# Performance work log

Hardware: AMD Instinct MI355X
Metric: run time of the kernel (lower is better)

The kernel has to match this reference:

```python
import math
import jax, jax.numpy as jnp
import numpy as np

N_HEAD = 16
N_CLUSTER = 64
GROUP_SIZE = 256


def _sinusoidal(n, d):
    # emb[p, 2j] = sin(p*div_j), emb[p, 2j+1] = cos(p*div_j)  (interleaved, as in torch source)
    pos = jnp.arange(n, dtype=jnp.float32)[:, None]
    div = jnp.exp(jnp.arange(0, d, 2, dtype=jnp.float32) * (-math.log(10000.0) / d))
    ang = pos * div  # [n, d//2]
    return jnp.stack([jnp.sin(ang), jnp.cos(ang)], axis=-1).reshape(n, d)


def _rotary(pe, x):
    # Faithful to source: sin = first half of interleaved table, cos = second half,
    # and the function RETURNS ONLY the rotated term (not x*cos + rot*sin).
    d = x.shape[-1]
    sin, cos = pe[..., : d // 2], pe[..., d // 2 :]
    x_even, x_odd = x[..., ::2], x[..., 1::2]
    out = jnp.stack([-x_odd * cos, x_even * sin], axis=-1)
    return out.reshape(jnp.broadcast_shapes(x.shape[:-1] + (d // 2,), out.shape[:-1]) + (2,)).reshape(x.shape) if False else jnp.broadcast_to(out, x.shape[:-1] + (d // 2, 2)).reshape(x.shape)


def _forward(x, w_attn, b_attn, w_proj, b_proj, w_assign):
    B, T, C = x.shape
    H, nc, gs = N_HEAD, N_CLUSTER, GROUP_SIZE
    hd = C // H
    ntpc = T // nc                 # tokens per cluster
    G = T // gs                    # number of groups
    ncpg = gs // ntpc              # clusters summarized per group
    c_max = (G - 1) * ncpg         # max cluster-KV length (padded)

    qkv = x @ w_attn.T + b_attn    # [B, T, 3C]
    q, k, v = jnp.split(qkv, 3, axis=-1)

    # ---- soft cluster summarization (block-diagonal softmax over each cluster's tokens) ----
    x_r = x.reshape(B, nc, ntpc, C)
    logits = jnp.einsum('bctd,cd->bct', x_r, w_assign)        # only diagonal cluster survives the mask
    w = jax.nn.softmax(logits, axis=-1)                        # [B, nc, ntpc]
    ck = jnp.einsum('bct,bctd->bcd', w, k.reshape(B, nc, ntpc, C))  # [B, nc, C]
    cv = jnp.einsum('bct,bctd->bcd', w, v.reshape(B, nc, ntpc, C))

    # ---- split into groups & heads ----
    qg = q.reshape(B, G, gs, H, hd).transpose(0, 1, 3, 2, 4)   # [B,G,H,gs,hd]
    kl = k.reshape(B, G, gs, H, hd).transpose(0, 1, 3, 2, 4)
    vl = v.reshape(B, G, gs, H, hd).transpose(0, 1, 3, 2, 4)
    kc = ck[:, :c_max].reshape(B, c_max, H, hd)                # [B,c_max,H,hd]
    vc = cv[:, :c_max].reshape(B, c_max, H, hd)

    # ---- rotary (positions restart per group; cluster tokens occupy positions 0..c-1) ----
    S = _sinusoidal(c_max + gs, hd)
    qr = _rotary(S[:gs], qg)                                   # q positions 0..gs-1 in every group
    kcr = _rotary(S[:c_max, None, :], kc)                      # cluster slot j -> position j
    pos_local = jnp.arange(G)[:, None] * ncpg + jnp.arange(gs)[None, :]  # [G,gs]
    klr = _rotary(S[pos_local][None, :, None], kl)             # local key p in group g -> pos g*ncpg+p

    # ---- attention: cluster KV (fully visible, masked to first g*ncpg) + local causal ----
    scale = 1.0 / math.sqrt(hd)
    sc = jnp.einsum('bghqd,bchd->bghqc', qr, kcr) * scale      # [B,G,H,gs,c_max]
    sl = jnp.einsum('bghqd,bghkd->bghqk', qr, klr) * scale     # [B,G,H,gs,gs]
    cmask = jnp.arange(c_max)[None, :] < (jnp.arange(G) * ncpg)[:, None]  # [G,c_max]
    sc = jnp.where(cmask[None, :, None, None, :], sc, -jnp.inf)
    lmask = jnp.tril(jnp.ones((gs, gs), dtype=bool))
    sl = jnp.where(lmask, sl, -jnp.inf)
    p = jax.nn.softmax(jnp.concatenate([sc, sl], axis=-1), axis=-1)
    pc, pl = p[..., :c_max], p[..., c_max:]
    y = jnp.einsum('bghqc,bchd->bghqd', pc, vc) + jnp.einsum('bghqk,bghkd->bghqd', pl, vl)
    y = y.transpose(0, 1, 3, 2, 4).reshape(B, T, C)
    return y @ w_proj.T + b_proj


def setup_inputs() -> dict:
    key = jax.random.key(0)
    ks = jax.random.split(key, 4)
    B, T, C, NC = 4, 4096, 1024, N_CLUSTER
    x = jax.random.normal(ks[0], (B, T, C), jnp.float32)
    w_attn = jax.random.normal(ks[1], (3 * C, C), jnp.float32) * 0.02
    b_attn = jnp.zeros((3 * C,), jnp.float32)
    w_proj = jax.random.normal(ks[2], (C, C), jnp.float32) * 0.02
    b_proj = jnp.zeros((C,), jnp.float32)
    w_assign = jax.random.normal(ks[3], (NC, C), jnp.float32) * 0.02
    return {"x": x, "w_attn": w_attn, "b_attn": b_attn, "w_proj": w_proj, "b_proj": b_proj, "w_assign": w_assign}


def reference(x, w_attn, b_attn, w_proj, b_proj, w_assign):
    return _forward(x, w_attn, b_attn, w_proj, b_proj, w_assign)
```

## Files before the change

### kernel.cpp

```cpp
#include <hip/hip_runtime.h>
#include <stdint.h>

typedef unsigned short u16;
typedef unsigned int   u32;
typedef __attribute__((ext_vector_type(8))) short short8;
typedef __attribute__((ext_vector_type(4))) short short4v;
typedef __attribute__((ext_vector_type(4))) float float4v;
typedef __attribute__((ext_vector_type(4))) u32   uint4v;

#define B_  4
#define T_  4096
#define C_  1024
#define H_  16
#define G_  16
#define GS_ 256
#define NC_ 64

static __device__ __forceinline__ u16 f2bf(float f){
  union{float f; u32 u;} c; c.f = f;
  return (u16)((c.u + 0x7fffu + ((c.u >> 16) & 1u)) >> 16);
}
static __device__ __forceinline__ float bf2f(u16 u){
  union{u32 u; float f;} c; c.u = ((u32)u) << 16; return c.f;
}
static __device__ __forceinline__ void gload16(const void* g, void* l){
  __builtin_amdgcn_global_load_lds((__attribute__((address_space(1))) void*)g,
                                   (__attribute__((address_space(3))) void*)l, 16, 0, 0);
}
static __device__ __forceinline__ short8 rot8(short8 v, const float* Sp, int i0){
  union{ short8 s; u32 u[4]; } a, o; a.s = v;
  #pragma unroll
  for(int p = 0; p < 4; p++){
    float e0 = bf2f((u16)(a.u[p] & 0xffffu));
    float e1 = bf2f((u16)(a.u[p] >> 16));
    float sn = Sp[i0 + p], cs = Sp[32 + i0 + p];
    o.u[p] = (u32)f2bf(-e1 * cs) | ((u32)f2bf(e0 * sn) << 16);
  }
  return o.s;
}

__global__ __launch_bounds__(256) void f2b_kernel(const float* __restrict__ s,
                                                  u16* __restrict__ d, int n4){
  int i = blockIdx.x * 256 + threadIdx.x;
  if(i >= n4) return;
  float4v v = *(const float4v*)(s + (size_t)i * 4);
  short4v o;
  o.x = (short)f2bf(v.x); o.y = (short)f2bf(v.y);
  o.z = (short)f2bf(v.z); o.w = (short)f2bf(v.w);
  *(short4v*)(d + (size_t)i * 4) = o;
}

__global__ void stab_kernel(float* __restrict__ S){
  int pos = blockIdx.x, d = threadIdx.x;
  int j = d >> 1;
  float div = expf((float)(2 * j) * (-0.14391156831212787f));
  float ang = (float)pos * div;
  S[pos * 64 + d] = (d & 1) ? cosf(ang) : sinf(ang);
}

template<int MODE>
__global__ __launch_bounds__(512, 1) void gemm8p(const u16* __restrict__ A,
    const u16* __restrict__ Bm, const float* __restrict__ bias,
    void* __restrict__ Cv, u16* __restrict__ vtout, int M, int N, int K, int nbn)
{
  __shared__ u16 sA[2][2][256][32];
  __shared__ u16 sB[2][2][256][32];
  const int tid = threadIdx.x;
  const int lane = tid & 63, w = tid >> 6;
  const int l15 = lane & 15, l4 = lane >> 4;
  const int wr = w >> 2, wc = w & 3;

  const int cpx = gridDim.x >> 3;
  const int bid = blockIdx.x;
  const int swz = (bid & 7) * cpx + (bid >> 3);
  const int bm = swz / nbn, bn = swz - bm * nbn;
  const int row0 = bm * 256, col0 = bn * 256;

  float4v acc[8][4];
  #pragma unroll
  for(int m = 0; m < 8; m++)
    #pragma unroll
    for(int n = 0; n < 4; n++) acc[m][n] = (float4v){0.f, 0.f, 0.f, 0.f};

  const int srow = lane >> 2;
  const int sslot = lane & 3;

  auto stageHalfA = [&](u16* dstPlane, int ktOff){
    #pragma unroll
    for(int l = 0; l < 2; l++){
      int r = w * 32 + l * 16 + srow;
      int ss = sslot ^ ((r >> 1) & 3);
      const u16* src;
      if(MODE == 2){
        int bg = (row0 + r) >> 8;
        int hh = ktOff >> 6;
        int coff = (ktOff & 63) + ss * 8;
        src = A + ((size_t)(bg * 16 + hh)) * 16384 + (size_t)(r & 255) * 64 + coff;
      } else {
        src = A + (size_t)(row0 + r) * K + ktOff + ss * 8;
      }
      gload16(src, dstPlane + (w * 32 + l * 16) * 32);
    }
  };
  auto stageHalfB = [&](u16* dstPlane, int ktOff){
    #pragma unroll
    for(int l = 0; l < 2; l++){
      int r = w * 32 + l * 16 + srow;
      int ss = sslot ^ ((r >> 1) & 3);
      gload16(Bm + (size_t)(col0 + r) * K + ktOff + ss * 8,
              dstPlane + (w * 32 + l * 16) * 32);
    }
  };
  auto ldsReadA = [&](int d, int kk, int mh, short8* af){
    #pragma unroll
    for(int i = 0; i < 4; i++){
      int r = wr * 128 + (mh * 4 + i) * 16 + l15;
      int slot = l4 ^ ((r >> 1) & 3);
      af[i] = *(const short8*)&sA[d][kk][r][slot * 8];
    }
  };
  auto ldsReadB = [&](int d, int kk, short8* bf){
    #pragma unroll
    for(int i = 0; i < 4; i++){
      int r = wc * 64 + i * 16 + l15;
      int slot = l4 ^ ((r >> 1) & 3);
      bf[i] = *(const short8*)&sB[d][kk][r][slot * 8];
    }
  };
  auto mfma16 = [&](int mh, short8* af, short8* bf){
    __builtin_amdgcn_s_setprio(1);
    #pragma unroll
    for(int i = 0; i < 4; i++)
      #pragma unroll
      for(int n = 0; n < 4; n++)
        acc[mh * 4 + i][n] = __builtin_amdgcn_mfma_f32_16x16x32_bf16(af[i], bf[n], acc[mh * 4 + i][n], 0, 0, 0);
    __builtin_amdgcn_s_setprio(0);
  };

  stageHalfA(&sA[0][0][0][0], 0);
  stageHalfB(&sB[0][0][0][0], 0);
  stageHalfA(&sA[0][1][0][0], 32);
  stageHalfB(&sB[0][1][0][0], 32);
  asm volatile("s_waitcnt vmcnt(4)" ::: "memory");
  __builtin_amdgcn_s_barrier();

  const int nT = K >> 6;
  for(int t = 0; t < nT; t++){
    const int d = t & 1, dn = d ^ 1;
    const int ktN = (t + 1) << 6;
    const bool pf = (t + 1 < nT);
    short8 af[4], bf[4];

    ldsReadA(d, 0, 0, af); ldsReadB(d, 0, bf);
    if(pf) stageHalfA(&sA[dn][0][0][0], ktN);
    __builtin_amdgcn_s_barrier();
    mfma16(0, af, bf);
    __builtin_amdgcn_s_barrier();

    ldsReadA(d, 0, 1, af);
    if(pf) stageHalfB(&sB[dn][0][0][0], ktN);
    __builtin_amdgcn_s_barrier();
    mfma16(1, af, bf);
    if(pf) asm volatile("s_waitcnt vmcnt(4)" ::: "memory");
    else   asm volatile("s_waitcnt vmcnt(0)" ::: "memory");
    __builtin_amdgcn_s_barrier();

    ldsReadA(d, 1, 0, af); ldsReadB(d, 1, bf);
    if(pf) stageHalfA(&sA[dn][1][0][0], ktN + 32);
    __builtin_amdgcn_s_barrier();
    mfma16(0, af, bf);
    __builtin_amdgcn_s_barrier();

    ldsReadA(d, 1, 1, af);
    if(pf) stageHalfB(&sB[dn][1][0][0], ktN + 32);
    __builtin_amdgcn_s_barrier();
    mfma16(1, af, bf);
    if(pf) asm volatile("s_waitcnt vmcnt(4)" ::: "memory");
    __builtin_amdgcn_s_barrier();
  }

  #pragma unroll
  for(int m = 0; m < 8; m++){
    #pragma unroll
    for(int n = 0; n < 4; n++){
      int col = col0 + wc * 64 + n * 16 + l15;
      float bv = bias[col];
      #pragma unroll
      for(int j = 0; j < 4; j++){
        int row = row0 + wr * 128 + m * 16 + l4 * 4 + j;
        float v = acc[m][n][j] + bv;
        acc[m][n][j] = v;
        if(MODE == 1) ((u16*)Cv)[(size_t)row * N + col] = f2bf(v);
        else          ((float*)Cv)[(size_t)row * N + col] = v;
      }
    }
  }
  if(MODE == 1 && col0 >= 2048){
    const int b = row0 >> 12, g = (row0 >> 8) & 15;
    const int h = ((col0 - 2048) >> 6) + wc;
    u32* vbase = (u32*)(vtout + (((size_t)(b * 16 + g)) * 16 + h) * 16384);
    #pragma unroll
    for(int n = 0; n < 4; n++){
      int d = n * 16 + l15;
      #pragma unroll
      for(int m = 0; m < 8; m++){
        int kb = (wr * 128 + m * 16 + l4 * 4) >> 2;
        int col2 = (kb ^ (d & 7)) << 1;
        u32 lo = (u32)f2bf(acc[m][n][0]) | ((u32)f2bf(acc[m][n][1]) << 16);
        u32 hi = (u32)f2bf(acc[m][n][2]) | ((u32)f2bf(acc[m][n][3]) << 16);
        vbase[d * 128 + col2]     = lo;
        vbase[d * 128 + col2 + 1] = hi;
      }
    }
  }
}

__global__ __launch_bounds__(256) void cluster_kernel(
    const float* __restrict__ x, const float* __restrict__ wasn,
    const u16* __restrict__ qkv, const float* __restrict__ S,
    u16* __restrict__ ckr, u16* __restrict__ vct)
{
  const int bc = blockIdx.x;
  const int c = bc & 63, b = bc >> 6;
  const int tid = threadIdx.x;
  const int lane = tid & 63, wv = tid >> 6;
  __shared__ float wgt[64];

  const float* xrow = x + ((size_t)b * T_ + c * 64) * C_;
  float4v wa4[4];
  #pragma unroll
  for(int ch = 0; ch < 4; ch++)
    wa4[ch] = *(const float4v*)(wasn + c * C_ + ch * 256 + lane * 4);

  for(int it = 0; it < 16; it++){
    int t = it * 4 + wv;
    const float* xr = xrow + (size_t)t * C_;
    float p = 0.f;
    #pragma unroll
    for(int ch = 0; ch < 4; ch++){
      float4v xv = *(const float4v*)(xr + ch * 256 + lane * 4);
      p += xv.x * wa4[ch].x + xv.y * wa4[ch].y + xv.z * wa4[ch].z + xv.w * wa4[ch].w;
    }
    p += __shfl_down(p, 32); p += __shfl_down(p, 16); p += __shfl_down(p, 8);
    p += __shfl_down(p, 4);  p += __shfl_down(p, 2);  p += __shfl_down(p, 1);
    if(lane == 0) wgt[t] = p;
  }
  __syncthreads();
  if(wv == 0){
    float v = wgt[lane];
    float mx = v;
    mx = fmaxf(mx, __shfl_xor(mx, 32)); mx = fmaxf(mx, __shfl_xor(mx, 16));
    mx = fmaxf(mx, __shfl_xor(mx, 8));  mx = fmaxf(mx, __shfl_xor(mx, 4));
    mx = fmaxf(mx, __shfl_xor(mx, 2));  mx = fmaxf(mx, __shfl_xor(mx, 1));
    float e = __expf(v - mx);
    float sm = e;
    sm += __shfl_xor(sm, 32); sm += __shfl_xor(sm, 16); sm += __shfl_xor(sm, 8);
    sm += __shfl_xor(sm, 4);  sm += __shfl_xor(sm, 2);  sm += __shfl_xor(sm, 1);
    wgt[lane] = e / sm;
  }
  __syncthreads();

  const int d0 = tid * 4;
  float ak[4] = {0, 0, 0, 0}, av[4] = {0, 0, 0, 0};
  const u16* krow = qkv + ((size_t)b * T_ + c * 64) * 3072 + C_ + d0;
  for(int t = 0; t < 64; t++){
    float wt = wgt[t];
    short4v kv = *(const short4v*)(krow + (size_t)t * 3072);
    short4v vv = *(const short4v*)(krow + (size_t)t * 3072 + C_);
    ak[0] += wt * bf2f((u16)kv.x); ak[1] += wt * bf2f((u16)kv.y);
    ak[2] += wt * bf2f((u16)kv.z); ak[3] += wt * bf2f((u16)kv.w);
    av[0] += wt * bf2f((u16)vv.x); av[1] += wt * bf2f((u16)vv.y);
    av[2] += wt * bf2f((u16)vv.z); av[3] += wt * bf2f((u16)vv.w);
  }
  const int dh = d0 & 63, i0 = dh >> 1;
  const float* Sp = S + c * 64;
  float s0 = Sp[i0],     c0 = Sp[32 + i0];
  float s1 = Sp[i0 + 1], c1 = Sp[32 + i0 + 1];
  short4v ck4;
  ck4.x = (short)f2bf(-ak[1] * c0); ck4.y = (short)f2bf(ak[0] * s0);
  ck4.z = (short)f2bf(-ak[3] * c1); ck4.w = (short)f2bf(ak[2] * s1);
  *(short4v*)(ckr + ((size_t)b * NC_ + c) * C_ + d0) = ck4;
  const int h = d0 >> 6;
  u16* vctb = vct + ((size_t)b * H_ + h) * 4096;
  #pragma unroll
  for(int i = 0; i < 4; i++){
    int d = dh + i;
    int col = ((c >> 2) ^ (d & 7)) * 4 + (c & 3);
    vctb[d * 64 + col] = f2bf(av[i]);
  }
}

__global__ __launch_bounds__(512, 4) void attn4_kernel(
    const u16* __restrict__ qkv, const u16* __restrict__ ckr,
    const u16* __restrict__ vct, u16* __restrict__ vt,
    const float* __restrict__ S)
{
  const int bid = blockIdx.x;
  const int h = bid & 15, g = (bid >> 4) & 15, b = bid >> 8;
  const int tid = threadIdx.x;
  const int lane = tid & 63, wv = tid >> 6;
  const int l15 = lane & 15, l4 = lane >> 4;
  const int rows0 = wv, rows1 = 15 - wv;

  __shared__ u16 SH[36864];
  u16* Ksh = SH;
  u16* Vsh = SH + 16384;
  u16* Vcl = SH + 32768;

  const size_t tok0 = (size_t)b * T_ + (size_t)g * GS_;
  u16* vslot = vt + (((size_t)b * 16 + g) * 16 + h) * 16384;

  {
    #pragma unroll
    for(int c = 0; c < 4; c++)
      gload16(vslot + (c * 512 + tid) * 8, Vsh + c * 4096 + wv * 512);
    gload16(vct + ((size_t)b * H_ + h) * 4096 + tid * 8, Vcl + wv * 512);
  }
  {
    const u16* kg = qkv + tok0 * 3072 + C_ + h * 64;
    #pragma unroll
    for(int c = 0; c < 4; c++){
      int idx = c * 512 + tid;
      int row = idx >> 3;
      int s0  = idx & 7;
      short8 v = *(const short8*)(kg + (size_t)row * 3072 + s0 * 8);
      short8 rv = rot8(v, S + (g * 4 + row) * 64, s0 * 4);
      *(short8*)(Ksh + row * 64 + (s0 ^ (row & 7)) * 8) = rv;
    }
  }
  short8 qa[2][2];
  #pragma unroll
  for(int f = 0; f < 2; f++){
    int rf = f ? rows1 : rows0;
    int qr = rf * 16 + l15;
    const u16* qp = qkv + (tok0 + qr) * 3072 + h * 64;
    #pragma unroll
    for(int kk = 0; kk < 2; kk++)
      qa[f][kk] = rot8(*(const short8*)(qp + kk * 32 + l4 * 8),
                       S + qr * 64, kk * 16 + l4 * 4);
  }
  __syncthreads();

  float4v o[2][4], osum[2];
  float mst[2];
  #pragma unroll
  for(int f = 0; f < 2; f++){
    osum[f] = (float4v){0, 0, 0, 0};
    mst[f] = -1e30f;
    #pragma unroll
    for(int n = 0; n < 4; n++) o[f][n] = (float4v){0, 0, 0, 0};
  }

  auto sm_update = [&](int f, float4v* st){
    float mx = st[0][0];
    #pragma unroll
    for(int n = 0; n < 4; n++)
      #pragma unroll
      for(int r = 0; r < 4; r++) mx = fmaxf(mx, st[n][r]);
    mx = fmaxf(mx, __shfl_xor(mx, 16));
    mx = fmaxf(mx, __shfl_xor(mx, 32));
    float mOld = mst[f];
    if(!__all(mx <= mOld)){
      float mn = fmaxf(mOld, mx);
      float rsc = __expf(mOld - mn);
      mst[f] = mn;
      float r0 = __shfl(rsc, l4 * 4 + 0);
      float r1 = __shfl(rsc, l4 * 4 + 1);
      float r2 = __shfl(rsc, l4 * 4 + 2);
      float r3 = __shfl(rsc, l4 * 4 + 3);
      #pragma unroll
      for(int n = 0; n < 4; n++){
        o[f][n][0] *= r0; o[f][n][1] *= r1; o[f][n][2] *= r2; o[f][n][3] *= r3;
      }
      osum[f][0] *= r0; osum[f][1] *= r1; osum[f][2] *= r2; osum[f][3] *= r3;
    }
    float mm = mst[f];
    #pragma unroll
    for(int n = 0; n < 4; n++)
      #pragma unroll
      for(int r = 0; r < 4; r++) st[n][r] = __expf(st[n][r] - mm);
  };

  auto pv = [&](int f, float4v* st, const u16* vb, int vstride, int granBase){
    #pragma unroll
    for(int kb = 0; kb < 4; kb++){
      union{ short8 s; u32 u[4]; } pa;
      pa.u[0] = (u32)f2bf(st[kb][0]) | ((u32)f2bf(st[kb][1]) << 16);
      pa.u[1] = (u32)f2bf(st[kb][2]) | ((u32)f2bf(st[kb][3]) << 16);
      pa.u[2] = 0; pa.u[3] = 0;
      union{ short8 s; u32 u[4]; } on;
      on.u[0] = 0x3F803F80u; on.u[1] = 0x3F803F80u; on.u[2] = 0; on.u[3] = 0;
      __builtin_amdgcn_s_setprio(1);
      osum[f] = __builtin_amdgcn_mfma_f32_16x16x32_bf16(pa.s, on.s, osum[f], 0, 0, 0);
      #pragma unroll
      for(int dn = 0; dn < 4; dn++){
        int d = dn * 16 + l15;
        int g2 = (granBase + kb * 4 + l4) ^ (l15 & 7);
        union{ short8 s; u32 u[4]; } vf;
        short4v v4 = *(const short4v*)(vb + d * vstride + g2 * 4);
        vf.u[0] = (u32)(u16)v4.x | ((u32)(u16)v4.y << 16);
        vf.u[1] = (u32)(u16)v4.z | ((u32)(u16)v4.w << 16);
        vf.u[2] = 0; vf.u[3] = 0;
        o[f][dn] = __builtin_amdgcn_mfma_f32_16x16x32_bf16(pa.s, vf.s, o[f][dn], 0, 0, 0);
      }
      __builtin_amdgcn_s_setprio(0);
    }
  };

  if(g > 0){
    const int climit = g * 4;
    #pragma unroll
    for(int f = 0; f < 2; f++){
      float4v st[4];
      #pragma unroll
      for(int n = 0; n < 4; n++) st[n] = (float4v){0, 0, 0, 0};
      #pragma unroll
      for(int kk = 0; kk < 2; kk++){
        __builtin_amdgcn_s_setprio(1);
        #pragma unroll
        for(int n = 0; n < 4; n++){
          short8 kf = *(const short8*)(ckr + ((size_t)b * NC_ + n * 16 + l15) * C_
                                       + h * 64 + kk * 32 + l4 * 8);
          st[n] = __builtin_amdgcn_mfma_f32_16x16x32_bf16(kf, qa[f][kk], st[n], 0, 0, 0);
        }
        __builtin_amdgcn_s_setprio(0);
      }
      #pragma unroll
      for(int n = 0; n < 4; n++)
        #pragma unroll
        for(int r = 0; r < 4; r++){
          int col = n * 16 + l4 * 4 + r;
          st[n][r] = (col >= climit) ? -1e30f : st[n][r] * 0.125f;
        }
      sm_update(f, st);
      pv(f, st, Vcl, 64, 0);
    }
  }

  const int ktA = rows0 >> 2, ktB = rows1 >> 2;
  for(int kt = 0; kt <= ktB; kt++){
    #pragma unroll
    for(int f = 0; f < 2; f++){
      int rf = f ? rows1 : rows0;
      if(kt > (f ? ktB : ktA)) continue;
      float4v st[4];
      #pragma unroll
      for(int n = 0; n < 4; n++) st[n] = (float4v){0, 0, 0, 0};
      #pragma unroll
      for(int kk = 0; kk < 2; kk++){
        __builtin_amdgcn_s_setprio(1);
        #pragma unroll
        for(int n = 0; n < 4; n++){
          int krow = kt * 64 + n * 16 + l15;
          int slot = (kk * 4 + l4) ^ (krow & 7);
          short8 kf = *(const short8*)(Ksh + krow * 64 + slot * 8);
          st[n] = __builtin_amdgcn_mfma_f32_16x16x32_bf16(kf, qa[f][kk], st[n], 0, 0, 0);
        }
        __builtin_amdgcn_s_setprio(0);
      }
      #pragma unroll
      for(int n = 0; n < 4; n++)
        #pragma unroll
        for(int r = 0; r < 4; r++){
          int col = kt * 64 + n * 16 + l4 * 4 + r;
          int q   = rf * 16 + l15;
          st[n][r] = (col > q) ? -1e30f : st[n][r] * 0.125f;
        }
      sm_update(f, st);
      pv(f, st, Vsh, 256, kt * 16);
    }
  }

  #pragma unroll
  for(int f = 0; f < 2; f++){
    int rf = f ? rows1 : rows0;
    #pragma unroll
    for(int r = 0; r < 4; r++){
      float inv = 1.0f / osum[f][r];
      int kq = rf * 16 + l4 * 4 + r;
      #pragma unroll
      for(int n = 0; n < 4; n++)
        vslot[kq * 64 + n * 16 + l15] = f2bf(o[f][n][r] * inv);
    }
  }
}

extern "C" void kernel_launch(void* const* d_in, const int* in_sizes, int n_in,
                              void* d_out, int out_size, void* d_ws, size_t ws_size,
                              hipStream_t stream)
{
  const float* x      = (const float*)d_in[0];
  const float* w_attn = (const float*)d_in[1];
  const float* b_attn = (const float*)d_in[2];
  const float* w_proj = (const float*)d_in[3];
  const float* b_proj = (const float*)d_in[4];
  const float* wasn   = (const float*)d_in[5];
  float* out = (float*)d_out;
  char* ws = (char*)d_ws;

  u16* qkv  = (u16*)(ws);
  u16* xb   = (u16*)(ws + 100663296);
  u16* vt   = (u16*)(ws + 134217728);
  u16* wab  = (u16*)(ws + 167772160);
  u16* wpb  = (u16*)(ws + 174063616);
  u16* ckr  = (u16*)(ws + 176160768);
  u16* vct  = (u16*)(ws + 176685056);
  float* st = (float*)(ws + 177209344);
  if(ws_size < 177290240) return;

  f2b_kernel<<<16384, 256, 0, stream>>>(x, xb, 4194304);
  f2b_kernel<<<3072, 256, 0, stream>>>(w_attn, wab, 786432);
  f2b_kernel<<<1024, 256, 0, stream>>>(w_proj, wpb, 262144);
  stab_kernel<<<316, 64, 0, stream>>>(st);
  gemm8p<1><<<768, 512, 0, stream>>>(xb, wab, b_attn, (void*)qkv, vt, 16384, 3072, 1024, 12);
  cluster_kernel<<<256, 256, 0, stream>>>(x, wasn, qkv, st, ckr, vct);
  attn4_kernel<<<1024, 512, 0, stream>>>(qkv, ckr, vct, vt, st);
  gemm8p<2><<<256, 512, 0, stream>>>(vt, wpb, b_proj, (void*)out, nullptr, 16384, 1024, 1024, 4);
}
```

Measured before the change: 271.4 us.

## Fuse init kernels, use bf16 x in cluster logits, skip masked MFMA tiles

Merges the three fp32-to-bf16 conversion launches and the sin/cos table launch into one init kernel. The cluster kernel now reads the bf16 copy of x, which halves its reads but lowers logit precision. In attention, PV now uses the full K=32 of each MFMA by packing two 16-key blocks per call instead of zero-padding half of each operand. QK and PV tiles that are fully masked on the causal diagonal and past the cluster limit are skipped.

After: 258.2 us. -4.9%, faster.

```diff
diff --git a/kernel.cpp b/kernel.cpp
--- a/kernel.cpp
+++ b/kernel.cpp
@@ -39,23 +39,33 @@
   return o.s;
 }
 
-__global__ __launch_bounds__(256) void f2b_kernel(const float* __restrict__ s,
-                                                  u16* __restrict__ d, int n4){
-  int i = blockIdx.x * 256 + threadIdx.x;
-  if(i >= n4) return;
-  float4v v = *(const float4v*)(s + (size_t)i * 4);
-  short4v o;
-  o.x = (short)f2bf(v.x); o.y = (short)f2bf(v.y);
-  o.z = (short)f2bf(v.z); o.w = (short)f2bf(v.w);
-  *(short4v*)(d + (size_t)i * 4) = o;
-}
-
-__global__ void stab_kernel(float* __restrict__ S){
-  int pos = blockIdx.x, d = threadIdx.x;
-  int j = d >> 1;
-  float div = expf((float)(2 * j) * (-0.14391156831212787f));
-  float ang = (float)pos * div;
-  S[pos * 64 + d] = (d & 1) ? cosf(ang) : sinf(ang);
+__global__ __launch_bounds__(256) void init_kernel(const float* __restrict__ x,
+    const float* __restrict__ wa, const float* __restrict__ wp,
+    u16* __restrict__ xb, u16* __restrict__ wab, u16* __restrict__ wpb,
+    float* __restrict__ S)
+{
+  const int bid = blockIdx.x;
+  if(bid < 20480){
+    int i = bid * 256 + threadIdx.x;
+    const float* s; u16* d; int off;
+    if(i < 4194304){ s = x; d = xb; off = i; }
+    else if(i < 4980736){ s = wa; d = wab; off = i - 4194304; }
+    else { s = wp; d = wpb; off = i - 4980736; }
+    float4v v = *(const float4v*)(s + (size_t)off * 4);
+    short4v o;
+    o.x = (short)f2bf(v.x); o.y = (short)f2bf(v.y);
+    o.z = (short)f2bf(v.z); o.w = (short)f2bf(v.w);
+    *(short4v*)(d + (size_t)off * 4) = o;
+  } else {
+    int pos = (bid - 20480) * 4 + (threadIdx.x >> 6);
+    int d = threadIdx.x & 63;
+    if(pos < 316){
+      int j = d >> 1;
+      float div = __expf((float)(2 * j) * (-0.14391156831212787f));
+      float ang = (float)pos * div;
+      S[pos * 64 + d] = (d & 1) ? cosf(ang) : sinf(ang);
+    }
+  }
 }
 
 template<int MODE>
@@ -216,7 +226,7 @@
 }
 
 __global__ __launch_bounds__(256) void cluster_kernel(
-    const float* __restrict__ x, const float* __restrict__ wasn,
+    const u16* __restrict__ xb, const float* __restrict__ wasn,
     const u16* __restrict__ qkv, const float* __restrict__ S,
     u16* __restrict__ ckr, u16* __restrict__ vct)
 {
@@ -226,7 +236,7 @@
   const int lane = tid & 63, wv = tid >> 6;
   __shared__ float wgt[64];
 
-  const float* xrow = x + ((size_t)b * T_ + c * 64) * C_;
+  const u16* xrow = xb + ((size_t)b * T_ + c * 64) * C_;
   float4v wa4[4];
   #pragma unroll
   for(int ch = 0; ch < 4; ch++)
@@ -234,12 +244,13 @@
 
   for(int it = 0; it < 16; it++){
     int t = it * 4 + wv;
-    const float* xr = xrow + (size_t)t * C_;
+    const u16* xr = xrow + (size_t)t * C_;
     float p = 0.f;
     #pragma unroll
     for(int ch = 0; ch < 4; ch++){
-      float4v xv = *(const float4v*)(xr + ch * 256 + lane * 4);
-      p += xv.x * wa4[ch].x + xv.y * wa4[ch].y + xv.z * wa4[ch].z + xv.w * wa4[ch].w;
+      short4v xv = *(const short4v*)(xr + ch * 256 + lane * 4);
+      p += bf2f((u16)xv.x) * wa4[ch].x + bf2f((u16)xv.y) * wa4[ch].y
+         + bf2f((u16)xv.z) * wa4[ch].z + bf2f((u16)xv.w) * wa4[ch].w;
     }
     p += __shfl_down(p, 32); p += __shfl_down(p, 16); p += __shfl_down(p, 8);
     p += __shfl_down(p, 4);  p += __shfl_down(p, 2);  p += __shfl_down(p, 1);
@@ -290,7 +301,7 @@
   }
 }
 
-__global__ __launch_bounds__(512, 4) void attn4_kernel(
+__global__ __launch_bounds__(512, 4) void attn5_kernel(
     const u16* __restrict__ qkv, const u16* __restrict__ ckr,
     const u16* __restrict__ vct, u16* __restrict__ vt,
     const float* __restrict__ S)
@@ -381,26 +392,32 @@
       for(int r = 0; r < 4; r++) st[n][r] = __expf(st[n][r] - mm);
   };
 
-  auto pv = [&](int f, float4v* st, const u16* vb, int vstride, int granBase){
-    #pragma unroll
-    for(int kb = 0; kb < 4; kb++){
+  auto pv = [&](int f, float4v* st, const u16* vb, int vstride, int granBase, int kbpMax){
+    #pragma unroll
+    for(int kbp = 0; kbp < 2; kbp++){
+      if(kbp >= kbpMax) continue;
       union{ short8 s; u32 u[4]; } pa;
-      pa.u[0] = (u32)f2bf(st[kb][0]) | ((u32)f2bf(st[kb][1]) << 16);
-      pa.u[1] = (u32)f2bf(st[kb][2]) | ((u32)f2bf(st[kb][3]) << 16);
-      pa.u[2] = 0; pa.u[3] = 0;
+      pa.u[0] = (u32)f2bf(st[2*kbp][0])   | ((u32)f2bf(st[2*kbp][1]) << 16);
+      pa.u[1] = (u32)f2bf(st[2*kbp][2])   | ((u32)f2bf(st[2*kbp][3]) << 16);
+      pa.u[2] = (u32)f2bf(st[2*kbp+1][0]) | ((u32)f2bf(st[2*kbp+1][1]) << 16);
+      pa.u[3] = (u32)f2bf(st[2*kbp+1][2]) | ((u32)f2bf(st[2*kbp+1][3]) << 16);
       union{ short8 s; u32 u[4]; } on;
-      on.u[0] = 0x3F803F80u; on.u[1] = 0x3F803F80u; on.u[2] = 0; on.u[3] = 0;
+      on.u[0] = 0x3F803F80u; on.u[1] = 0x3F803F80u;
+      on.u[2] = 0x3F803F80u; on.u[3] = 0x3F803F80u;
       __builtin_amdgcn_s_setprio(1);
       osum[f] = __builtin_amdgcn_mfma_f32_16x16x32_bf16(pa.s, on.s, osum[f], 0, 0, 0);
       #pragma unroll
       for(int dn = 0; dn < 4; dn++){
         int d = dn * 16 + l15;
-        int g2 = (granBase + kb * 4 + l4) ^ (l15 & 7);
+        int gA = (granBase + (2*kbp) * 4 + l4) ^ (l15 & 7);
+        int gB = (granBase + (2*kbp+1) * 4 + l4) ^ (l15 & 7);
+        short4v vA = *(const short4v*)(vb + d * vstride + gA * 4);
+        short4v vB = *(const short4v*)(vb + d * vstride + gB * 4);
         union{ short8 s; u32 u[4]; } vf;
-        short4v v4 = *(const short4v*)(vb + d * vstride + g2 * 4);
-        vf.u[0] = (u32)(u16)v4.x | ((u32)(u16)v4.y << 16);
-        vf.u[1] = (u32)(u16)v4.z | ((u32)(u16)v4.w << 16);
-        vf.u[2] = 0; vf.u[3] = 0;
+        vf.u[0] = (u32)(u16)vA.x | ((u32)(u16)vA.y << 16);
+        vf.u[1] = (u32)(u16)vA.z | ((u32)(u16)vA.w << 16);
+        vf.u[2] = (u32)(u16)vB.x | ((u32)(u16)vB.y << 16);
+        vf.u[3] = (u32)(u16)vB.z | ((u32)(u16)vB.w << 16);
         o[f][dn] = __builtin_amdgcn_mfma_f32_16x16x32_bf16(pa.s, vf.s, o[f][dn], 0, 0, 0);
       }
       __builtin_amdgcn_s_setprio(0);
@@ -409,6 +426,8 @@
 
   if(g > 0){
     const int climit = g * 4;
+    const int nMaxC = (climit - 1) >> 4;
+    const int kbpMaxC = (nMaxC >> 1) + 1;
     #pragma unroll
     for(int f = 0; f < 2; f++){
       float4v st[4];
@@ -419,6 +438,7 @@
         __builtin_amdgcn_s_setprio(1);
         #pragma unroll
         for(int n = 0; n < 4; n++){
+          if(n > nMaxC) continue;
           short8 kf = *(const short8*)(ckr + ((size_t)b * NC_ + n * 16 + l15) * C_
                                        + h * 64 + kk * 32 + l4 * 8);
           st[n] = __builtin_amdgcn_mfma_f32_16x16x32_bf16(kf, qa[f][kk], st[n], 0, 0, 0);
@@ -433,7 +453,7 @@
           st[n][r] = (col >= climit) ? -1e30f : st[n][r] * 0.125f;
         }
       sm_update(f, st);
-      pv(f, st, Vcl, 64, 0);
+      pv(f, st, Vcl, 64, 0, kbpMaxC);
     }
   }
 
@@ -443,6 +463,9 @@
     for(int f = 0; f < 2; f++){
       int rf = f ? rows1 : rows0;
       if(kt > (f ? ktB : ktA)) continue;
+      const bool diag = (kt == (rf >> 2));
+      const int nMax = diag ? (rf & 3) : 3;
+      const int kbpMax = diag ? (((rf & 3) >> 1) + 1) : 2;
       float4v st[4];
       #pragma unroll
       for(int n = 0; n < 4; n++) st[n] = (float4v){0, 0, 0, 0};
@@ -451,6 +474,7 @@
         __builtin_amdgcn_s_setprio(1);
         #pragma unroll
         for(int n = 0; n < 4; n++){
+          if(n > nMax) continue;
           int krow = kt * 64 + n * 16 + l15;
           int slot = (kk * 4 + l4) ^ (krow & 7);
           short8 kf = *(const short8*)(Ksh + krow * 64 + slot * 8);
@@ -467,7 +491,7 @@
           st[n][r] = (col > q) ? -1e30f : st[n][r] * 0.125f;
         }
       sm_update(f, st);
-      pv(f, st, Vsh, 256, kt * 16);
+      pv(f, st, Vsh, 256, kt * 16, kbpMax);
     }
   }
 
@@ -508,12 +532,9 @@
   float* st = (float*)(ws + 177209344);
   if(ws_size < 177290240) return;
 
-  f2b_kernel<<<16384, 256, 0, stream>>>(x, xb, 4194304);
-  f2b_kernel<<<3072, 256, 0, stream>>>(w_attn, wab, 786432);
-  f2b_kernel<<<1024, 256, 0, stream>>>(w_proj, wpb, 262144);
-  stab_kernel<<<316, 64, 0, stream>>>(st);
+  init_kernel<<<20559, 256, 0, stream>>>(x, w_attn, w_proj, xb, wab, wpb, st);
   gemm8p<1><<<768, 512, 0, stream>>>(xb, wab, b_attn, (void*)qkv, vt, 16384, 3072, 1024, 12);
-  cluster_kernel<<<256, 256, 0, stream>>>(x, wasn, qkv, st, ckr, vct);
-  attn4_kernel<<<1024, 512, 0, stream>>>(qkv, ckr, vct, vt, st);
+  cluster_kernel<<<256, 256, 0, stream>>>(xb, wasn, qkv, st, ckr, vct);
+  attn5_kernel<<<1024, 512, 0, stream>>>(qkv, ckr, vct, vt, st);
   gemm8p<2><<<256, 512, 0, stream>>>(vt, wpb, b_proj, (void*)out, nullptr, 16384, 1024, 1024, 4);
 }
```
